# Performance work log

Hardware: AMD Instinct MI355X
Metric: run time of the kernel (lower is better)

Reference implementation:

```python
import jax, jax.numpy as jnp
import numpy as np

SINKHORN_NUM_ITERS = 50   # from LearnablePermutation.sinkhorn_num_iters
SINKHORN_TEMP = 0.1       # from LearnablePermutation.sinkhorn_temp
GUMBEL_NOISE_STD = 1.0    # gumbel_noise_std when training_module is None
N = 64                    # num_features
B = 8192                  # batch_size


def setup_inputs() -> dict:
    key = jax.random.key(0)
    k1, k2 = jax.random.split(key)
    gamma = jax.random.normal(k1, (N, N), dtype=jnp.float32)
    # Pre-sampled Gumbel-like noise (stand-in for sample_gumbel_noise) so the
    # reference is deterministic; the Sinkhorn math is identical.
    gumbel_noise = jax.random.normal(k2, (B, N, N), dtype=jnp.float32)
    return {"gamma": gamma, "gumbel_noise": gumbel_noise}


def reference(gamma, gumbel_noise):
    # parameterized_gamma for permutation_type='soft': -logsigmoid(gamma)
    gamma_p = -jax.nn.log_sigmoid(gamma)                      # [N, N]
    noise = gumbel_noise * GUMBEL_NOISE_STD                   # [B, N, N]
    log_alpha = (gamma_p[None, :, :] + noise) / SINKHORN_TEMP # [B, N, N]

    def sinkhorn_step(la, _):
        la = la - jax.nn.logsumexp(la, axis=-1, keepdims=True)  # row normalize
        la = la - jax.nn.logsumexp(la, axis=-2, keepdims=True)  # col normalize
        return la, None

    log_alpha, _ = jax.lax.scan(sinkhorn_step, log_alpha, None,
                                length=SINKHORN_NUM_ITERS)
    return jnp.exp(log_alpha)  # doubly-stochastic soft permutation matrices [B, N, N]
```

## Files before the change

### kernel.cpp

```cpp
#include <hip/hip_runtime.h>


#define L2E   1.4426950408889634f
#define SCALE 14.426950408889634f
#define NITER 50

template<int CTRL>
__device__ __forceinline__ float dppmov(float x) {
  return __int_as_float(__builtin_amdgcn_update_dpp(
      0, __float_as_int(x), CTRL, 0xF, 0xF, true));
}

__device__ __forceinline__ float swz_x16(float x) {
  return __int_as_float(__builtin_amdgcn_ds_swizzle(__float_as_int(x), 0x401F));
}
__device__ __forceinline__ float bperm(int addr, float x) {
  return __int_as_float(__builtin_amdgcn_ds_bpermute(addr, __float_as_int(x)));
}

__global__ __launch_bounds__(256) void sinkhorn64(
    const float* __restrict__ gamma,
    const float* __restrict__ noise,
    float* __restrict__ out, int batch) {
  const int lane = threadIdx.x & 63;
  const int m = blockIdx.x * 4 + (threadIdx.x >> 6);
  if (m >= batch) return;

  const int lr = lane >> 3;
  const int lc = lane & 7;
  const int tile_off = (lr * 8) * 64 + lc * 8;
  const float* src  = noise + (size_t)m * 4096 + tile_off;
  const float* gsrc = gamma + tile_off;
  const int addr32 = (lane ^ 32) << 2;

  float a[8][8];

#pragma unroll
  for (int i = 0; i < 8; ++i) {
    const float4 n0 = *(const float4*)(src + i * 64);
    const float4 n1 = *(const float4*)(src + i * 64 + 4);
    const float4 g0 = *(const float4*)(gsrc + i * 64);
    const float4 g1 = *(const float4*)(gsrc + i * 64 + 4);
    const float nv[8] = {n0.x, n0.y, n0.z, n0.w, n1.x, n1.y, n1.z, n1.w};
    const float gv[8] = {g0.x, g0.y, g0.z, g0.w, g1.x, g1.y, g1.z, g1.w};
#pragma unroll
    for (int j = 0; j < 8; ++j) {
      float gp = 10.0f * __builtin_amdgcn_logf(1.0f + __builtin_amdgcn_exp2f(-gv[j] * L2E));
      a[i][j] = fmaf(nv[j], SCALE, gp);
    }
  }

#pragma unroll
  for (int i = 0; i < 8; ++i) {
    float mx = fmaxf(fmaxf(fmaxf(a[i][0], a[i][1]), fmaxf(a[i][2], a[i][3])),
                     fmaxf(fmaxf(a[i][4], a[i][5]), fmaxf(a[i][6], a[i][7])));
    mx = fmaxf(mx, dppmov<0xB1>(mx));
    mx = fmaxf(mx, dppmov<0x4E>(mx));
    mx = fmaxf(mx, dppmov<0x141>(mx));
#pragma unroll
    for (int j = 0; j < 8; ++j)
      a[i][j] = __builtin_amdgcn_exp2f(a[i][j] - mx);
  }

  float u[8], v[8];
#pragma unroll
  for (int j = 0; j < 8; ++j) v[j] = 1.0f;

#pragma unroll 1
  for (int it = 0; it < NITER; ++it) {
#pragma unroll
    for (int i = 0; i < 8; ++i) {
      float s = a[i][0] * v[0];
#pragma unroll
      for (int j = 1; j < 8; ++j) s = fmaf(a[i][j], v[j], s);
      s += dppmov<0xB1>(s);
      s += dppmov<0x4E>(s);
      s += dppmov<0x141>(s);
      u[i] = __builtin_amdgcn_rcpf(s);
    }
#pragma unroll
    for (int j = 0; j < 8; ++j) {
      float s = a[0][j] * u[0];
#pragma unroll
      for (int i = 1; i < 8; ++i) s = fmaf(a[i][j], u[i], s);
      s += dppmov<0x128>(s);
      s += swz_x16(s);
      s += bperm(addr32, s);
      v[j] = __builtin_amdgcn_rcpf(s);
    }
  }

  float* dst = out + (size_t)m * 4096 + tile_off;
#pragma unroll
  for (int i = 0; i < 8; ++i) {
    const float ui = u[i];
    float o[8];
#pragma unroll
    for (int j = 0; j < 8; ++j) o[j] = a[i][j] * ui * v[j];
    *(float4*)(dst + i * 64)     = make_float4(o[0], o[1], o[2], o[3]);
    *(float4*)(dst + i * 64 + 4) = make_float4(o[4], o[5], o[6], o[7]);
  }
}

extern "C" void kernel_launch(void* const* d_in, const int* in_sizes, int n_in,
                              void* d_out, int out_size, void* d_ws, size_t ws_size,
                              hipStream_t stream) {
  const float* gamma = (const float*)d_in[0];
  const float* noise = (const float*)d_in[1];
  float* out = (float*)d_out;
  const int batch = in_sizes[1] / 4096;
  const int blocks = (batch + 3) / 4;
  sinkhorn64<<<blocks, 256, 0, stream>>>(gamma, noise, out, batch);
}
```

Before: 330.8 us.

## Use packed FP32 math, precompute gamma transform in workspace, raise occupancy

The main Sinkhorn loop now uses two-wide float vectors so the compiler can emit packed FMA/mul instructions (v_pk_fma_f32) for the row and column reductions. The -logsigmoid(gamma) transform moves into a separate small kernel that writes to workspace when it is available, so each wave no longer evaluates exp/log per element. Launch bounds now request 3 blocks per CU. The trade-offs are an extra kernel launch and possible register pressure or spills from the occupancy hint on the 64-register tile.

Measured after the change: 313.5 us. 5.2% less time.

```diff
diff --git a/kernel.cpp b/kernel.cpp
--- a/kernel.cpp
+++ b/kernel.cpp
@@ -1,5 +1,7 @@
 #include <hip/hip_runtime.h>
 
+
+typedef float v2f __attribute__((ext_vector_type(2)));
 
 #define L2E   1.4426950408889634f
 #define SCALE 14.426950408889634f
@@ -18,7 +20,15 @@
   return __int_as_float(__builtin_amdgcn_ds_bpermute(addr, __float_as_int(x)));
 }
 
-__global__ __launch_bounds__(256) void sinkhorn64(
+__global__ __launch_bounds__(256) void prep_gp(const float* __restrict__ g,
+                                               float* __restrict__ gp) {
+  const int i = blockIdx.x * 256 + threadIdx.x;
+  const float x = g[i];
+  gp[i] = 10.0f * __builtin_amdgcn_logf(1.0f + __builtin_amdgcn_exp2f(-x * L2E));
+}
+
+__global__ __launch_bounds__(256, 3) void sinkhorn64(
+    const float* __restrict__ gp,
     const float* __restrict__ gamma,
     const float* __restrict__ noise,
     float* __restrict__ out, int batch) {
@@ -29,76 +39,103 @@
   const int lr = lane >> 3;
   const int lc = lane & 7;
   const int tile_off = (lr * 8) * 64 + lc * 8;
-  const float* src  = noise + (size_t)m * 4096 + tile_off;
-  const float* gsrc = gamma + tile_off;
+  const float* src = noise + (size_t)m * 4096 + tile_off;
   const int addr32 = (lane ^ 32) << 2;
 
-  float a[8][8];
+  v2f a2[8][4];
 
 #pragma unroll
   for (int i = 0; i < 8; ++i) {
     const float4 n0 = *(const float4*)(src + i * 64);
     const float4 n1 = *(const float4*)(src + i * 64 + 4);
-    const float4 g0 = *(const float4*)(gsrc + i * 64);
-    const float4 g1 = *(const float4*)(gsrc + i * 64 + 4);
-    const float nv[8] = {n0.x, n0.y, n0.z, n0.w, n1.x, n1.y, n1.z, n1.w};
-    const float gv[8] = {g0.x, g0.y, g0.z, g0.w, g1.x, g1.y, g1.z, g1.w};
+    const v2f n2[4] = {{n0.x, n0.y}, {n0.z, n0.w}, {n1.x, n1.y}, {n1.z, n1.w}};
+    v2f g2[4];
+    if (gp) {
+      const float4 g0 = *(const float4*)(gp + tile_off + i * 64);
+      const float4 g1 = *(const float4*)(gp + tile_off + i * 64 + 4);
+      g2[0] = (v2f){g0.x, g0.y}; g2[1] = (v2f){g0.z, g0.w};
+      g2[2] = (v2f){g1.x, g1.y}; g2[3] = (v2f){g1.z, g1.w};
+    } else {
+      const float4 g0 = *(const float4*)(gamma + tile_off + i * 64);
+      const float4 g1 = *(const float4*)(gamma + tile_off + i * 64 + 4);
+      const float gv[8] = {g0.x, g0.y, g0.z, g0.w, g1.x, g1.y, g1.z, g1.w};
+      float gq[8];
 #pragma unroll
-    for (int j = 0; j < 8; ++j) {
-      float gp = 10.0f * __builtin_amdgcn_logf(1.0f + __builtin_amdgcn_exp2f(-gv[j] * L2E));
-      a[i][j] = fmaf(nv[j], SCALE, gp);
+      for (int j = 0; j < 8; ++j)
+        gq[j] = 10.0f * __builtin_amdgcn_logf(1.0f + __builtin_amdgcn_exp2f(-gv[j] * L2E));
+      g2[0] = (v2f){gq[0], gq[1]}; g2[1] = (v2f){gq[2], gq[3]};
+      g2[2] = (v2f){gq[4], gq[5]}; g2[3] = (v2f){gq[6], gq[7]};
     }
+    const v2f sc2 = {SCALE, SCALE};
+#pragma unroll
+    for (int jj = 0; jj < 4; ++jj)
+      a2[i][jj] = __builtin_elementwise_fma(n2[jj], sc2, g2[jj]);
   }
 
 #pragma unroll
   for (int i = 0; i < 8; ++i) {
-    float mx = fmaxf(fmaxf(fmaxf(a[i][0], a[i][1]), fmaxf(a[i][2], a[i][3])),
-                     fmaxf(fmaxf(a[i][4], a[i][5]), fmaxf(a[i][6], a[i][7])));
+    v2f m2 = __builtin_elementwise_max(
+        __builtin_elementwise_max(a2[i][0], a2[i][1]),
+        __builtin_elementwise_max(a2[i][2], a2[i][3]));
+    float mx = fmaxf(m2.x, m2.y);
     mx = fmaxf(mx, dppmov<0xB1>(mx));
     mx = fmaxf(mx, dppmov<0x4E>(mx));
     mx = fmaxf(mx, dppmov<0x141>(mx));
+    const v2f mx2 = {mx, mx};
 #pragma unroll
-    for (int j = 0; j < 8; ++j)
-      a[i][j] = __builtin_amdgcn_exp2f(a[i][j] - mx);
+    for (int jj = 0; jj < 4; ++jj) {
+      const v2f d = a2[i][jj] - mx2;
+      a2[i][jj] = (v2f){__builtin_amdgcn_exp2f(d.x), __builtin_amdgcn_exp2f(d.y)};
+    }
   }
 
-  float u[8], v[8];
+  v2f vv[4];
 #pragma unroll
-  for (int j = 0; j < 8; ++j) v[j] = 1.0f;
+  for (int jj = 0; jj < 4; ++jj) vv[jj] = (v2f){1.0f, 1.0f};
+  float u[8];
 
 #pragma unroll 1
   for (int it = 0; it < NITER; ++it) {
 #pragma unroll
     for (int i = 0; i < 8; ++i) {
-      float s = a[i][0] * v[0];
-#pragma unroll
-      for (int j = 1; j < 8; ++j) s = fmaf(a[i][j], v[j], s);
+      v2f s2 = a2[i][0] * vv[0];
+      s2 = __builtin_elementwise_fma(a2[i][1], vv[1], s2);
+      s2 = __builtin_elementwise_fma(a2[i][2], vv[2], s2);
+      s2 = __builtin_elementwise_fma(a2[i][3], vv[3], s2);
+      float s = s2.x + s2.y;
       s += dppmov<0xB1>(s);
       s += dppmov<0x4E>(s);
       s += dppmov<0x141>(s);
       u[i] = __builtin_amdgcn_rcpf(s);
     }
+    v2f ub[8];
 #pragma unroll
-    for (int j = 0; j < 8; ++j) {
-      float s = a[0][j] * u[0];
+    for (int i = 0; i < 8; ++i) ub[i] = (v2f){u[i], u[i]};
 #pragma unroll
-      for (int i = 1; i < 8; ++i) s = fmaf(a[i][j], u[i], s);
-      s += dppmov<0x128>(s);
-      s += swz_x16(s);
-      s += bperm(addr32, s);
-      v[j] = __builtin_amdgcn_rcpf(s);
+    for (int jj = 0; jj < 4; ++jj) {
+      v2f s2 = a2[0][jj] * ub[0];
+#pragma unroll
+      for (int i = 1; i < 8; ++i) s2 = __builtin_elementwise_fma(a2[i][jj], ub[i], s2);
+      float sx = s2.x, sy = s2.y;
+      sx += dppmov<0x128>(sx);
+      sx += swz_x16(sx);
+      sx += bperm(addr32, sx);
+      sy += dppmov<0x128>(sy);
+      sy += swz_x16(sy);
+      sy += bperm(addr32, sy);
+      vv[jj] = (v2f){__builtin_amdgcn_rcpf(sx), __builtin_amdgcn_rcpf(sy)};
     }
   }
 
   float* dst = out + (size_t)m * 4096 + tile_off;
 #pragma unroll
   for (int i = 0; i < 8; ++i) {
-    const float ui = u[i];
-    float o[8];
+    const v2f ui2 = (v2f){u[i], u[i]};
+    v2f o2[4];
 #pragma unroll
-    for (int j = 0; j < 8; ++j) o[j] = a[i][j] * ui * v[j];
-    *(float4*)(dst + i * 64)     = make_float4(o[0], o[1], o[2], o[3]);
-    *(float4*)(dst + i * 64 + 4) = make_float4(o[4], o[5], o[6], o[7]);
+    for (int jj = 0; jj < 4; ++jj) o2[jj] = a2[i][jj] * ui2 * vv[jj];
+    *(float4*)(dst + i * 64)     = make_float4(o2[0].x, o2[0].y, o2[1].x, o2[1].y);
+    *(float4*)(dst + i * 64 + 4) = make_float4(o2[2].x, o2[2].y, o2[3].x, o2[3].y);
   }
 }
 
@@ -110,5 +147,11 @@
   float* out = (float*)d_out;
   const int batch = in_sizes[1] / 4096;
   const int blocks = (batch + 3) / 4;
-  sinkhorn64<<<blocks, 256, 0, stream>>>(gamma, noise, out, batch);
+
+  float* gp = nullptr;
+  if (ws_size >= 4096 * sizeof(float)) {
+    gp = (float*)d_ws;
+    prep_gp<<<16, 256, 0, stream>>>(gamma, gp);
+  }
+  sinkhorn64<<<blocks, 256, 0, stream>>>(gp, gamma, noise, out, batch);
 }
```
